# Kernel tuning notes

Measured on AMD Instinct MI355X. Metric: run time of the kernel, lower is better.

Reference implementation:

```python
import jax, jax.numpy as jnp
import numpy as np

# simulation params from inputs_cell = (dt, (gamma, omega, n, eta, kappa, b), trainable_params)
DT = 1e-3
GAMMA = 0.3
NBAR = 2.0
ETA = 0.8
KAPPA = 0.9
B, T = 512, 4096


def setup_inputs() -> dict:
    key = jax.random.key(0)
    k1, = jax.random.split(key, 1)
    # measurement increments dy ~ sqrt(dt)-scaled noise, shape [B, T, 2]
    dy = jax.random.normal(k1, (B, T, 2), dtype=jnp.float32) * jnp.float32(np.sqrt(DT))
    # state = (<q>, <p>, Var[q], Var[p], Cov(q,p), t); start at vacuum-ish cov 0.5
    state0 = jnp.concatenate(
        [
            jnp.zeros((B, 2), jnp.float32),            # x
            0.5 * jnp.ones((B, 1), jnp.float32),       # vx
            0.5 * jnp.ones((B, 1), jnp.float32),       # vp
            jnp.zeros((B, 1), jnp.float32),            # cxp
            jnp.zeros((B, 1), jnp.float32),            # t
        ],
        axis=1,
    )
    omega_p = jnp.ones((1,), dtype=jnp.float32)  # trainable_params = 1.0
    return {"dy": dy, "state0": state0, "omega_p": omega_p}


def reference(dy, state0, omega_p):
    C = jnp.float32(np.sqrt(4.0 * ETA * KAPPA)) * jnp.array([[1.0, 0.0], [0.0, 0.0]], jnp.float32)
    D = jnp.float32(GAMMA * (NBAR + 0.5) + KAPPA) * jnp.eye(2, dtype=jnp.float32)
    J = jnp.array([[0.0, 1.0], [-1.0, 0.0]], jnp.float32)
    A = -0.5 * GAMMA * jnp.eye(2, dtype=jnp.float32) + omega_p[0] * J  # [2,2]

    dy_t_major = jnp.swapaxes(dy, 0, 1)  # [T, B, 2]

    def step(state, dy_t):
        x = state[:, :2]                                   # [B,2]
        vx, vp, cxp = state[:, 2], state[:, 3], state[:, 4]
        t = state[:, 5]
        cov = jnp.stack(
            [jnp.stack([vx, cxp], -1), jnp.stack([cxp, vp], -1)], -2
        )  # [B,2,2]
        xicov = jnp.einsum('bij,kj->bik', cov, C)          # cov @ C.T
        M = A - jnp.einsum('bij,jk->bik', xicov, C)        # A - xicov @ C
        dx = jnp.einsum('bij,bj->bi', M, x) * DT + jnp.einsum('bij,bj->bi', xicov, dy_t)
        dcov = DT * (
            jnp.einsum('bij,kj->bik', cov, A)              # cov @ A.T
            + jnp.einsum('ij,bjk->bik', A, cov)            # A @ cov
            + D
            - jnp.einsum('bij,bkj->bik', xicov, xicov)     # xicov @ xicov.T
        )
        ncov = cov + dcov
        nstate = jnp.concatenate(
            [x + dx, ncov[:, 0, 0:1], ncov[:, 1, 1:2], ncov[:, 1, 0:1], (t + DT)[:, None]],
            axis=1,
        )
        dy_hat = jnp.einsum('ij,bj->bi', C, x) * DT
        return nstate, dy_hat

    final_state, dy_hat = jax.lax.scan(step, state0, dy_t_major)
    return final_state, jnp.swapaxes(dy_hat, 0, 1)  # [B,6], [B,T,2]
```

## Files before the change

kernel.cpp:

```cpp
#include <hip/hip_runtime.h>
#include <math.h>


constexpr int T = 4096;
constexpr int B = 512;
constexpr int CH = 16;
constexpr int NC = T / CH;
constexpr int NSWEEP = 3;
constexpr int SB = 258;

__global__ __launch_bounds__(256) void grnn_fused(
    const float* __restrict__ dy,
    const float* __restrict__ state0,
    const float* __restrict__ omega_p,
    float* __restrict__ out)
{
    __shared__ float2 scovT[T];
    __shared__ float sbuf[CH * SB];
    __shared__ float4 sS[NC];
    __shared__ float wtotA[4][12];
    __shared__ float wtotX[4][6];
    const int b  = blockIdx.x;
    const int c  = threadIdx.x;
    const int l  = c & 63;
    const int wv = c >> 6;

    const float DT = 0.001f;
    const float w  = omega_p[0];
    const float k1 = 1.0f + DT * (-0.3f);
    const float k2 = DT * 2.0f * w;
    const float k3 = DT * 1.65f;
    const float k4 = DT * 2.88f;
    const float kw = DT * w;
    const float kA = 1.0f + DT * (-0.15f);
    const float cc = 1.69705627484771f;
    const float kcDT = cc * DT;
    const float nk4 = -k4, n2k4 = -2.0f * k4;
    const float w2c = 2.0f * w;

    const float* dyb = dy + (size_t)b * (T * 2);
    #pragma unroll
    for (int k = 0; k < 8; ++k) {
        const float4 d = *(const float4*)(dyb + 4 * (k * 256 + c));
        const int t0 = 2 * (k * 256 + c);
        const int j0 = t0 & 15;
        const int c0 = t0 >> 4;
        sbuf[j0 * SB + c0]       = d.x;
        sbuf[(j0 + 1) * SB + c0] = d.z;
    }

    float vx = state0[2], vp = state0[3], cx = state0[4];
    float S0 = vx, S1 = vp, S2 = cx;
    {
        const int Q = c >> 2, r = c & 3;
        const float dt64 = 64.0f * DT;
        for (int i = 0; i < 64; ++i) {
            if (i == Q) { S0 = vx; S1 = vp; S2 = cx; }
            const float fvx = fmaf(-2.88f, vx * vx, fmaf(-0.3f, vx, fmaf(w2c, cx, 1.65f)));
            const float fvp = fmaf(-2.88f, cx * cx, fmaf(-0.3f, vp, fmaf(-w2c, cx, 1.65f)));
            const float fcx = fmaf(-2.88f, vx * cx, fmaf(-0.3f, cx, w * (vp - vx)));
            vx = fmaf(dt64, fvx, vx);
            vp = fmaf(dt64, fvp, vp);
            cx = fmaf(dt64, fcx, cx);
        }
        vx = S0; vp = S1; cx = S2;
        const float dt16 = 16.0f * DT;
        #pragma unroll
        for (int i = 0; i < 3; ++i) {
            if (i < r) {
                const float fvx = fmaf(-2.88f, vx * vx, fmaf(-0.3f, vx, fmaf(w2c, cx, 1.65f)));
                const float fvp = fmaf(-2.88f, cx * cx, fmaf(-0.3f, vp, fmaf(-w2c, cx, 1.65f)));
                const float fcx = fmaf(-2.88f, vx * cx, fmaf(-0.3f, cx, w * (vp - vx)));
                vx = fmaf(dt16, fvx, vx);
                vp = fmaf(dt16, fvp, vp);
                cx = fmaf(dt16, fcx, cx);
            }
        }
        S0 = vx; S1 = vp; S2 = cx;
    }
    sS[c] = make_float4(S0, S1, S2, 0.f);
    __syncthreads();

    for (int sw = 0; sw < NSWEEP; ++sw) {
        float vx0 = S0, vp0 = S1, cx0 = S2;
        float m00=1.f,m01=0.f,m02=0.f, m10=0.f,m11=1.f,m12=0.f, m20=0.f,m21=0.f,m22=1.f;
        #pragma unroll 4
        for (int j = 0; j < CH; ++j) {
            const float J00 = fmaf(n2k4, vx0, k1);
            const float J12 = fmaf(n2k4, cx0, -k2);
            const float J20 = fmaf(nk4, cx0, -kw);
            const float J22 = fmaf(nk4, vx0, k1);
            const float a00 = fmaf(J00, m00, k2 * m20);
            const float a01 = fmaf(J00, m01, k2 * m21);
            const float a02 = fmaf(J00, m02, k2 * m22);
            const float a10 = fmaf(k1, m10, J12 * m20);
            const float a11 = fmaf(k1, m11, J12 * m21);
            const float a12 = fmaf(k1, m12, J12 * m22);
            const float a20 = fmaf(J20, m00, fmaf(kw, m10, J22 * m20));
            const float a21 = fmaf(J20, m01, fmaf(kw, m11, J22 * m21));
            const float a22 = fmaf(J20, m02, fmaf(kw, m12, J22 * m22));
            m00 = a00; m01 = a01; m02 = a02;
            m10 = a10; m11 = a11; m12 = a12;
            m20 = a20; m21 = a21; m22 = a22;
            const float t1   = fmaf(nk4, vx0, k1);
            const float s1   = fmaf(k2, cx0, k3);
            const float mvx  = -kw * vx0;
            const float mm   = fmaf(kw, vp0, mvx);
            const float cxp2 = cx0 * cx0;
            const float uu   = fmaf(-k2, cx0, k3);
            const float in2  = fmaf(nk4, cxp2, uu);
            const float nvp  = fmaf(k1, vp0, in2);
            const float nvx  = fmaf(t1, vx0, s1);
            const float ncx  = fmaf(t1, cx0, mm);
            vx0 = nvx; cx0 = ncx; vp0 = nvp;
        }
        const float4 Sn = sS[(c + 1) & (NC - 1)];
        float d0 = vx0 - Sn.x, d1 = vp0 - Sn.y, d2 = cx0 - Sn.z;
        if (c == NC - 1) { d0 = 0.f; d1 = 0.f; d2 = 0.f; }
        for (int k = 1; k < 64; k <<= 1) {
            const float o00 = __shfl_up(m00, k), o01 = __shfl_up(m01, k), o02 = __shfl_up(m02, k);
            const float o10 = __shfl_up(m10, k), o11 = __shfl_up(m11, k), o12 = __shfl_up(m12, k);
            const float o20 = __shfl_up(m20, k), o21 = __shfl_up(m21, k), o22 = __shfl_up(m22, k);
            const float e0  = __shfl_up(d0, k),  e1  = __shfl_up(d1, k),  e2  = __shfl_up(d2, k);
            if (l >= k) {
                const float b00 = fmaf(m00, o00, fmaf(m01, o10, m02 * o20));
                const float b01 = fmaf(m00, o01, fmaf(m01, o11, m02 * o21));
                const float b02 = fmaf(m00, o02, fmaf(m01, o12, m02 * o22));
                const float b10 = fmaf(m10, o00, fmaf(m11, o10, m12 * o20));
                const float b11 = fmaf(m10, o01, fmaf(m11, o11, m12 * o21));
                const float b12 = fmaf(m10, o02, fmaf(m11, o12, m12 * o22));
                const float b20 = fmaf(m20, o00, fmaf(m21, o10, m22 * o20));
                const float b21 = fmaf(m20, o01, fmaf(m21, o11, m22 * o21));
                const float b22 = fmaf(m20, o02, fmaf(m21, o12, m22 * o22));
                const float nd0 = fmaf(m00, e0, fmaf(m01, e1, fmaf(m02, e2, d0)));
                const float nd1 = fmaf(m10, e0, fmaf(m11, e1, fmaf(m12, e2, d1)));
                const float nd2 = fmaf(m20, e0, fmaf(m21, e1, fmaf(m22, e2, d2)));
                m00 = b00; m01 = b01; m02 = b02;
                m10 = b10; m11 = b11; m12 = b12;
                m20 = b20; m21 = b21; m22 = b22;
                d0 = nd0; d1 = nd1; d2 = nd2;
            }
        }
        if (l == 63) {
            float* wt = wtotA[wv];
            wt[0]=m00; wt[1]=m01; wt[2]=m02; wt[3]=m10; wt[4]=m11; wt[5]=m12;
            wt[6]=m20; wt[7]=m21; wt[8]=m22; wt[9]=d0; wt[10]=d1; wt[11]=d2;
        }
        __syncthreads();
        float pq0 = 0.f, pq1 = 0.f, pq2 = 0.f;
        for (int w2 = 0; w2 < wv; ++w2) {
            const float* wt = wtotA[w2];
            const float n0 = fmaf(wt[0],pq0,fmaf(wt[1],pq1,fmaf(wt[2],pq2,wt[9])));
            const float n1 = fmaf(wt[3],pq0,fmaf(wt[4],pq1,fmaf(wt[5],pq2,wt[10])));
            const float n2 = fmaf(wt[6],pq0,fmaf(wt[7],pq1,fmaf(wt[8],pq2,wt[11])));
            pq0 = n0; pq1 = n1; pq2 = n2;
        }
        const float qf0 = fmaf(m00,pq0,fmaf(m01,pq1,fmaf(m02,pq2,d0)));
        const float qf1 = fmaf(m10,pq0,fmaf(m11,pq1,fmaf(m12,pq2,d1)));
        const float qf2 = fmaf(m20,pq0,fmaf(m21,pq1,fmaf(m22,pq2,d2)));
        float E0 = __shfl_up(qf0, 1), E1 = __shfl_up(qf1, 1), E2 = __shfl_up(qf2, 1);
        if (l == 0) { E0 = pq0; E1 = pq1; E2 = pq2; }
        S0 += E0; S1 += E1; S2 += E2;
        __syncthreads();
        sS[c] = make_float4(S0, S1, S2, 0.f);
        __syncthreads();
    }

    float fvx = 0.f, fvp = 0.f, fcx = 0.f;
    {
        float vx0 = S0, vp0 = S1, cx0 = S2;
        #pragma unroll 4
        for (int j = 0; j < CH; ++j) {
            scovT[j * NC + c] = make_float2(vx0, cx0);
            const float t1   = fmaf(nk4, vx0, k1);
            const float s1   = fmaf(k2, cx0, k3);
            const float mvx  = -kw * vx0;
            const float mm   = fmaf(kw, vp0, mvx);
            const float cxp2 = cx0 * cx0;
            const float uu   = fmaf(-k2, cx0, k3);
            const float in2  = fmaf(nk4, cxp2, uu);
            const float nvp  = fmaf(k1, vp0, in2);
            const float nvx  = fmaf(t1, vx0, s1);
            const float ncx  = fmaf(t1, cx0, mm);
            vx0 = nvx; cx0 = ncx; vp0 = nvp;
        }
        fvx = vx0; fvp = vp0; fcx = cx0;
    }
    __syncthreads();

    float r00 = 1.f, r01 = 0.f, r10 = 0.f, r11 = 1.f;
    float q0 = 0.f, q1 = 0.f;
    #pragma unroll 4
    for (int j = CH - 1; j >= 0; --j) {
        const float2 vc = scovT[j * NC + c];
        const float d0v = sbuf[j * SB + c];
        const float T00 = fmaf(nk4, vc.x, kA);
        const float T10 = fmaf(nk4, vc.y, -kw);
        const float g0  = cc * vc.x;
        const float g1  = cc * vc.y;
        const float h0  = fmaf(r00, g0, r01 * g1);
        const float h1  = fmaf(r10, g0, r11 * g1);
        q0 = fmaf(h0, d0v, q0);
        q1 = fmaf(h1, d0v, q1);
        const float n00 = fmaf(r00, T00, r01 * T10);
        const float n01 = fmaf(r00, kw,  r01 * kA);
        const float n10 = fmaf(r10, T00, r11 * T10);
        const float n11 = fmaf(r10, kw,  r11 * kA);
        r00 = n00; r01 = n01; r10 = n10; r11 = n11;
    }
    float p00 = r00, p01 = r01, p10 = r10, p11 = r11;

    for (int d = 1; d < 64; d <<= 1) {
        const float o00 = __shfl_up(p00, d), o01 = __shfl_up(p01, d);
        const float o10 = __shfl_up(p10, d), o11 = __shfl_up(p11, d);
        const float oq0 = __shfl_up(q0, d),  oq1 = __shfl_up(q1, d);
        if (l >= d) {
            const float n00 = fmaf(p00, o00, p01 * o10);
            const float n01 = fmaf(p00, o01, p01 * o11);
            const float n10 = fmaf(p10, o00, p11 * o10);
            const float n11 = fmaf(p10, o01, p11 * o11);
            const float nq0 = fmaf(p00, oq0, fmaf(p01, oq1, q0));
            const float nq1 = fmaf(p10, oq0, fmaf(p11, oq1, q1));
            p00 = n00; p01 = n01; p10 = n10; p11 = n11;
            q0 = nq0; q1 = nq1;
        }
    }
    if (l == 63) {
        float* wt = wtotX[wv];
        wt[0] = p00; wt[1] = p01; wt[2] = p10; wt[3] = p11; wt[4] = q0; wt[5] = q1;
    }
    __syncthreads();
    float f00 = 1.f, f01 = 0.f, f10 = 0.f, f11 = 1.f, fq0 = 0.f, fq1 = 0.f;
    for (int w2 = 0; w2 < wv; ++w2) {
        const float* wt = wtotX[w2];
        const float t00 = wt[0], t01 = wt[1], t10 = wt[2], t11 = wt[3];
        const float tq0 = wt[4], tq1 = wt[5];
        const float n00 = fmaf(t00, f00, t01 * f10);
        const float n01 = fmaf(t00, f01, t01 * f11);
        const float n10 = fmaf(t10, f00, t11 * f10);
        const float n11 = fmaf(t10, f01, t11 * f11);
        const float nq0 = fmaf(t00, fq0, fmaf(t01, fq1, tq0));
        const float nq1 = fmaf(t10, fq0, fmaf(t11, fq1, tq1));
        f00 = n00; f01 = n01; f10 = n10; f11 = n11; fq0 = nq0; fq1 = nq1;
    }
    const float F00 = fmaf(p00, f00, p01 * f10);
    const float F01 = fmaf(p00, f01, p01 * f11);
    const float F10 = fmaf(p10, f00, p11 * f10);
    const float F11 = fmaf(p10, f01, p11 * f11);
    const float Fq0 = fmaf(p00, fq0, fmaf(p01, fq1, q0));
    const float Fq1 = fmaf(p10, fq0, fmaf(p11, fq1, q1));
    float e00 = __shfl_up(F00, 1), e01 = __shfl_up(F01, 1);
    float e10 = __shfl_up(F10, 1), e11 = __shfl_up(F11, 1);
    float eq0 = __shfl_up(Fq0, 1), eq1 = __shfl_up(Fq1, 1);
    if (l == 0) { e00 = f00; e01 = f01; e10 = f10; e11 = f11; eq0 = fq0; eq1 = fq1; }

    const float xi0 = state0[b * 6 + 0];
    const float xi1 = state0[b * 6 + 1];
    float x0 = fmaf(e00, xi0, fmaf(e01, xi1, eq0));
    float x1 = fmaf(e10, xi0, fmaf(e11, xi1, eq1));

    #pragma unroll 4
    for (int j = 0; j < CH; ++j) {
        const float2 vc = scovT[j * NC + c];
        const float d0v = sbuf[j * SB + c];
        const float T00 = fmaf(nk4, vc.x, kA);
        const float T10 = fmaf(nk4, vc.y, -kw);
        const float g0  = cc * vc.x;
        const float g1  = cc * vc.y;
        const float h0  = kcDT * x0;
        const float nx0 = fmaf(T00, x0, fmaf(kw, x1, g0 * d0v));
        const float nx1 = fmaf(T10, x0, fmaf(kA, x1, g1 * d0v));
        sbuf[j * SB + c] = h0;
        x0 = nx0; x1 = nx1;
    }

    if (c == NC - 1) {
        float* os = out + b * 6;
        os[0] = x0;  os[1] = x1;
        os[2] = fvx; os[3] = fvp; os[4] = fcx;
        os[5] = state0[5] + 4096.0f * 0.001f;
    }
    __syncthreads();

    float* dyh = out + B * 6 + (size_t)b * (T * 2);
    #pragma unroll
    for (int k = 0; k < 8; ++k) {
        const int t0 = 2 * (k * 256 + c);
        const int j0 = t0 & 15;
        const int c0 = t0 >> 4;
        const float h0 = sbuf[j0 * SB + c0];
        const float h1 = sbuf[(j0 + 1) * SB + c0];
        *(float4*)(dyh + 4 * (k * 256 + c)) = make_float4(h0, 0.f, h1, 0.f);
    }
}

extern "C" void kernel_launch(void* const* d_in, const int* in_sizes, int n_in,
                              void* d_out, int out_size, void* d_ws, size_t ws_size,
                              hipStream_t stream) {
    const float* dy     = (const float*)d_in[0];
    const float* state0 = (const float*)d_in[1];
    const float* omega  = (const float*)d_in[2];
    float* out = (float*)d_out;
    grnn_fused<<<B, 256, 0, stream>>>(dy, state0, omega, out);
}
```

Measured before the change: 92.62 us.

## Keep covariance trajectory in registers, cut sweeps, use shuffles for boundaries

Drops the shared-memory covariance trajectory and chunk-start arrays. Per-step covariances now live in fully unrolled register arrays, and neighbour chunk starts come from wave shuffles plus a small per-wave boundary table. The Newton-style sweep count falls from 3 to 2, and the coarse initial guess switches to 128-step strides with up to 7 refinement steps. The dy loads are issued into registers before the covariance precompute to hide their latency, and launch bounds ask for 2 blocks per CU. The cost is higher register pressure, and the lower sweep count risks accuracy if two sweeps do not converge.

New measurement: 85.08 us. 1.09x faster.

```diff
diff --git a/kernel.cpp b/kernel.cpp
--- a/kernel.cpp
+++ b/kernel.cpp
@@ -6,18 +6,17 @@
 constexpr int B = 512;
 constexpr int CH = 16;
 constexpr int NC = T / CH;
-constexpr int NSWEEP = 3;
+constexpr int NSWEEP = 2;
 constexpr int SB = 258;
 
-__global__ __launch_bounds__(256) void grnn_fused(
+__global__ __launch_bounds__(256, 2) void grnn_fused(
     const float* __restrict__ dy,
     const float* __restrict__ state0,
     const float* __restrict__ omega_p,
     float* __restrict__ out)
 {
-    __shared__ float2 scovT[T];
     __shared__ float sbuf[CH * SB];
-    __shared__ float4 sS[NC];
+    __shared__ float sBnd[4][3];
     __shared__ float wtotA[4][12];
     __shared__ float wtotX[4][6];
     const int b  = blockIdx.x;
@@ -39,34 +38,30 @@
     const float w2c = 2.0f * w;
 
     const float* dyb = dy + (size_t)b * (T * 2);
-    #pragma unroll
-    for (int k = 0; k < 8; ++k) {
-        const float4 d = *(const float4*)(dyb + 4 * (k * 256 + c));
-        const int t0 = 2 * (k * 256 + c);
-        const int j0 = t0 & 15;
-        const int c0 = t0 >> 4;
-        sbuf[j0 * SB + c0]       = d.x;
-        sbuf[(j0 + 1) * SB + c0] = d.z;
-    }
-
-    float vx = state0[2], vp = state0[3], cx = state0[4];
-    float S0 = vx, S1 = vp, S2 = cx;
+    float4 dreg[8];
+    #pragma unroll
+    for (int k = 0; k < 8; ++k)
+        dreg[k] = *(const float4*)(dyb + 4 * (k * 256 + c));
+
+    float S0, S1, S2;
     {
-        const int Q = c >> 2, r = c & 3;
-        const float dt64 = 64.0f * DT;
-        for (int i = 0; i < 64; ++i) {
+        const int Q = c >> 3, r = c & 7;
+        float vx = state0[2], vp = state0[3], cx = state0[4];
+        S0 = vx; S1 = vp; S2 = cx;
+        const float dt128 = 128.0f * DT;
+        for (int i = 0; i < 32; ++i) {
             if (i == Q) { S0 = vx; S1 = vp; S2 = cx; }
             const float fvx = fmaf(-2.88f, vx * vx, fmaf(-0.3f, vx, fmaf(w2c, cx, 1.65f)));
             const float fvp = fmaf(-2.88f, cx * cx, fmaf(-0.3f, vp, fmaf(-w2c, cx, 1.65f)));
             const float fcx = fmaf(-2.88f, vx * cx, fmaf(-0.3f, cx, w * (vp - vx)));
-            vx = fmaf(dt64, fvx, vx);
-            vp = fmaf(dt64, fvp, vp);
-            cx = fmaf(dt64, fcx, cx);
+            vx = fmaf(dt128, fvx, vx);
+            vp = fmaf(dt128, fvp, vp);
+            cx = fmaf(dt128, fcx, cx);
         }
         vx = S0; vp = S1; cx = S2;
         const float dt16 = 16.0f * DT;
         #pragma unroll
-        for (int i = 0; i < 3; ++i) {
+        for (int i = 0; i < 7; ++i) {
             if (i < r) {
                 const float fvx = fmaf(-2.88f, vx * vx, fmaf(-0.3f, vx, fmaf(w2c, cx, 1.65f)));
                 const float fvp = fmaf(-2.88f, cx * cx, fmaf(-0.3f, vp, fmaf(-w2c, cx, 1.65f)));
@@ -78,7 +73,16 @@
         }
         S0 = vx; S1 = vp; S2 = cx;
     }
-    sS[c] = make_float4(S0, S1, S2, 0.f);
+    if (l == 0) { sBnd[wv][0] = S0; sBnd[wv][1] = S1; sBnd[wv][2] = S2; }
+
+    #pragma unroll
+    for (int k = 0; k < 8; ++k) {
+        const int t0 = 2 * (k * 256 + c);
+        const int j0 = t0 & 15;
+        const int c0 = t0 >> 4;
+        sbuf[j0 * SB + c0]       = dreg[k].x;
+        sbuf[(j0 + 1) * SB + c0] = dreg[k].z;
+    }
     __syncthreads();
 
     for (int sw = 0; sw < NSWEEP; ++sw) {
@@ -114,8 +118,12 @@
             const float ncx  = fmaf(t1, cx0, mm);
             vx0 = nvx; cx0 = ncx; vp0 = nvp;
         }
-        const float4 Sn = sS[(c + 1) & (NC - 1)];
-        float d0 = vx0 - Sn.x, d1 = vp0 - Sn.y, d2 = cx0 - Sn.z;
+        float Sn0 = __shfl_down(S0, 1), Sn1 = __shfl_down(S1, 1), Sn2 = __shfl_down(S2, 1);
+        if (l == 63) {
+            const int wn = (wv < 3) ? wv + 1 : 3;
+            Sn0 = sBnd[wn][0]; Sn1 = sBnd[wn][1]; Sn2 = sBnd[wn][2];
+        }
+        float d0 = vx0 - Sn0, d1 = vp0 - Sn1, d2 = cx0 - Sn2;
         if (c == NC - 1) { d0 = 0.f; d1 = 0.f; d2 = 0.f; }
         for (int k = 1; k < 64; k <<= 1) {
             const float o00 = __shfl_up(m00, k), o01 = __shfl_up(m01, k), o02 = __shfl_up(m02, k);
@@ -161,17 +169,17 @@
         float E0 = __shfl_up(qf0, 1), E1 = __shfl_up(qf1, 1), E2 = __shfl_up(qf2, 1);
         if (l == 0) { E0 = pq0; E1 = pq1; E2 = pq2; }
         S0 += E0; S1 += E1; S2 += E2;
+        if (l == 0) { sBnd[wv][0] = S0; sBnd[wv][1] = S1; sBnd[wv][2] = S2; }
         __syncthreads();
-        sS[c] = make_float4(S0, S1, S2, 0.f);
-        __syncthreads();
-    }
-
-    float fvx = 0.f, fvp = 0.f, fcx = 0.f;
+    }
+
+    float sc0[CH], sc1[CH];
+    float fvx, fvp, fcx;
     {
         float vx0 = S0, vp0 = S1, cx0 = S2;
-        #pragma unroll 4
+        #pragma unroll
         for (int j = 0; j < CH; ++j) {
-            scovT[j * NC + c] = make_float2(vx0, cx0);
+            sc0[j] = vx0; sc1[j] = cx0;
             const float t1   = fmaf(nk4, vx0, k1);
             const float s1   = fmaf(k2, cx0, k3);
             const float mvx  = -kw * vx0;
@@ -186,18 +194,17 @@
         }
         fvx = vx0; fvp = vp0; fcx = cx0;
     }
-    __syncthreads();
 
     float r00 = 1.f, r01 = 0.f, r10 = 0.f, r11 = 1.f;
     float q0 = 0.f, q1 = 0.f;
-    #pragma unroll 4
+    #pragma unroll
     for (int j = CH - 1; j >= 0; --j) {
-        const float2 vc = scovT[j * NC + c];
+        const float vcx = sc0[j], vcc = sc1[j];
         const float d0v = sbuf[j * SB + c];
-        const float T00 = fmaf(nk4, vc.x, kA);
-        const float T10 = fmaf(nk4, vc.y, -kw);
-        const float g0  = cc * vc.x;
-        const float g1  = cc * vc.y;
+        const float T00 = fmaf(nk4, vcx, kA);
+        const float T10 = fmaf(nk4, vcc, -kw);
+        const float g0  = cc * vcx;
+        const float g1  = cc * vcc;
         const float h0  = fmaf(r00, g0, r01 * g1);
         const float h1  = fmaf(r10, g0, r11 * g1);
         q0 = fmaf(h0, d0v, q0);
@@ -259,14 +266,14 @@
     float x0 = fmaf(e00, xi0, fmaf(e01, xi1, eq0));
     float x1 = fmaf(e10, xi0, fmaf(e11, xi1, eq1));
 
-    #pragma unroll 4
+    #pragma unroll
     for (int j = 0; j < CH; ++j) {
-        const float2 vc = scovT[j * NC + c];
+        const float vcx = sc0[j], vcc = sc1[j];
         const float d0v = sbuf[j * SB + c];
-        const float T00 = fmaf(nk4, vc.x, kA);
-        const float T10 = fmaf(nk4, vc.y, -kw);
-        const float g0  = cc * vc.x;
-        const float g1  = cc * vc.y;
+        const float T00 = fmaf(nk4, vcx, kA);
+        const float T10 = fmaf(nk4, vcc, -kw);
+        const float g0  = cc * vcx;
+        const float g1  = cc * vcc;
         const float h0  = kcDT * x0;
         const float nx0 = fmaf(T00, x0, fmaf(kw, x1, g0 * d0v));
         const float nx1 = fmaf(T10, x0, fmaf(kA, x1, g1 * d0v));
```
